# Optimization experiments

Hardware: AMD Instinct MI355X
Metric: run time of the kernel (lower is better)

The kernel has to match this reference:

```python
import jax, jax.numpy as jnp
import numpy as np

N_NODES = 100000
N_EDGES = 1600000
HID = 128
N_GRAPHS = 512
MAX_Z = 1000
NODE_VOCAB = 200000
OUT = 2
BN_EPS = 1e-5


def setup_inputs() -> dict:
    key = jax.random.key(0)
    ks = jax.random.split(key, 20)

    def w(k, shape, fan_in):
        return jax.random.normal(k, shape, dtype=jnp.float32) / np.sqrt(fan_in)

    inp = {
        "num_nodes": N_NODES,
        "z": jax.random.randint(ks[0], (N_NODES,), 0, MAX_Z),
        "edge_index": jax.random.randint(ks[1], (2, N_EDGES), 0, N_NODES),
        "batch": jnp.sort(jax.random.randint(ks[2], (N_NODES,), 0, N_GRAPHS)),
        "node_id": jax.random.randint(ks[3], (N_NODES,), 0, NODE_VOCAB),
        # parameters
        "z_emb": jax.random.normal(ks[4], (MAX_Z, HID), dtype=jnp.float32) * 0.02,
        "node_emb": jax.random.normal(ks[5], (NODE_VOCAB, HID), dtype=jnp.float32) * 0.02,
        "W0": w(ks[6], (2 * HID, HID), 2 * HID), "b0": jnp.zeros((HID,), jnp.float32),
        "W1": w(ks[7], (HID, HID), HID), "b1": jnp.zeros((HID,), jnp.float32),
        "W2": w(ks[8], (HID, HID), HID), "b2": jnp.zeros((HID,), jnp.float32),
        "mlp_W1": w(ks[9], (HID, HID), HID), "mlp_b1": jnp.zeros((HID,), jnp.float32),
        "bn_gamma": jnp.ones((HID,), jnp.float32), "bn_beta": jnp.zeros((HID,), jnp.float32),
        "mlp_W2": w(ks[10], (HID, OUT), HID), "mlp_b2": jnp.zeros((OUT,), jnp.float32),
    }
    return inp


def _gin_conv(x, src, dst, W, b, num_nodes):
    # GINConv(eps=0): out_i = Linear(x_i + sum_{j->i} x_j)
    agg = jax.ops.segment_sum(x[src], dst, num_segments=num_nodes)
    return (x + agg) @ W + b


def reference(num_nodes, z, edge_index, batch, node_id,
              z_emb, node_emb, W0, b0, W1, b1, W2, b2,
              mlp_W1, mlp_b1, bn_gamma, bn_beta, mlp_W2, mlp_b2):
    src, dst = edge_index[0], edge_index[1]
    # node features: concat(z_embedding(z), node_embedding(node_id)) -> [N, 2H]
    x = jnp.concatenate([z_emb[z], node_emb[node_id]], axis=1)

    x = jax.nn.relu(_gin_conv(x, src, dst, W0, b0, num_nodes))  # [N, H]
    x = jax.nn.relu(_gin_conv(x, src, dst, W1, b1, num_nodes))
    x = _gin_conv(x, src, dst, W2, b2, num_nodes)  # last conv: no relu

    # global mean pool over graphs
    sums = jax.ops.segment_sum(x, batch, num_segments=N_GRAPHS)  # [G, H]
    counts = jax.ops.segment_sum(jnp.ones((num_nodes,), x.dtype), batch,
                                 num_segments=N_GRAPHS)
    pooled = sums / jnp.maximum(counts, 1.0)[:, None]

    # MLP([H, H, OUT]): Linear -> BatchNorm(eval, identity stats) -> ReLU -> Linear
    h = pooled @ mlp_W1 + mlp_b1
    h = h * (bn_gamma / np.sqrt(1.0 + BN_EPS)) + bn_beta
    h = jax.nn.relu(h)
    return h @ mlp_W2 + mlp_b2  # [G, OUT]
```

## Files before the change

kernel.cpp:

```cpp
#include <hip/hip_runtime.h>

#define NN 100000
#define NE 1600000
#define HID 128
#define NG 512
#define MAXZ 1000
#define NBK 256
#define BK_S 391
#define TILE_E 4096

typedef unsigned short u16;
typedef unsigned int u32;
typedef __attribute__((ext_vector_type(8))) short bf16x8;
typedef __attribute__((ext_vector_type(4))) float f32x4;

__device__ __forceinline__ u16 bf16r(float x) {
    u32 u = __float_as_uint(x);
    u32 r = (u + 0x7fffu + ((u >> 16) & 1u)) >> 16;
    return (u16)r;
}
__device__ __forceinline__ float bflo(u32 u) { return __uint_as_float(u << 16); }
__device__ __forceinline__ float bfhi(u32 u) { return __uint_as_float(u & 0xffff0000u); }

#define ACC8(v) { \
    acc[0] += bflo((v).x); acc[1] += bfhi((v).x); \
    acc[2] += bflo((v).y); acc[3] += bfhi((v).y); \
    acc[4] += bflo((v).z); acc[5] += bfhi((v).z); \
    acc[6] += bflo((v).w); acc[7] += bfhi((v).w); }

__global__ __launch_bounds__(256) void bucket_count_kernel(const int* __restrict__ dst,
                                                           int* __restrict__ bcount) {
    __shared__ int lh[NBK];
    int t = threadIdx.x;
    lh[t] = 0;
    __syncthreads();
    int stride = gridDim.x * 256;
    for (int i = blockIdx.x * 256 + t; i < NE; i += stride)
        atomicAdd(&lh[dst[i] / BK_S], 1);
    __syncthreads();
    int v = lh[t];
    if (v) atomicAdd(&bcount[t], v);
}

__global__ __launch_bounds__(NBK) void scan_nbk_kernel(const int* __restrict__ bcount,
                                                       int* __restrict__ boff,
                                                       int* __restrict__ gcursor) {
    __shared__ int buf[NBK];
    int t = threadIdx.x;
    int v = bcount[t];
    buf[t] = v;
    __syncthreads();
    for (int d = 1; d < NBK; d <<= 1) {
        int add = (t >= d) ? buf[t - d] : 0;
        __syncthreads();
        buf[t] += add;
        __syncthreads();
    }
    int excl = buf[t] - v;
    boff[t] = excl;
    gcursor[t] = excl;
    if (t == NBK - 1) boff[NBK] = buf[NBK - 1];
}

__global__ __launch_bounds__(256) void pair_scatter_kernel(const int* __restrict__ src,
                                                           const int* __restrict__ dst,
                                                           int* __restrict__ gcursor,
                                                           u32* __restrict__ pairs) {
    __shared__ int cnt[NBK];
    __shared__ int base[NBK];
    int t = threadIdx.x;
    long tile0 = (long)blockIdx.x * TILE_E;
    cnt[t] = 0;
    __syncthreads();
    u32 val[16], br[16];
#pragma unroll
    for (int i = 0; i < 16; ++i) {
        long idx = tile0 + i * 256 + t;
        val[i] = 0xFFFFFFFFu;
        if (idx < NE) {
            int d = dst[idx];
            int b = d / BK_S;
            int r = atomicAdd(&cnt[b], 1);
            val[i] = ((u32)(d - b * BK_S) << 17) | (u32)src[idx];
            br[i] = ((u32)b << 12) | (u32)r;
        }
    }
    __syncthreads();
    int c = cnt[t];
    if (c) base[t] = atomicAdd(&gcursor[t], c);
    __syncthreads();
#pragma unroll
    for (int i = 0; i < 16; ++i) {
        if (val[i] != 0xFFFFFFFFu) {
            u32 b = br[i] >> 12, r = br[i] & 0xFFFu;
            pairs[base[b] + r] = val[i];
        }
    }
}

__global__ __launch_bounds__(256) void bucket_build_kernel(const u32* __restrict__ pairs,
                                                           const int* __restrict__ boff,
                                                           int* __restrict__ off,
                                                           int* __restrict__ csr) {
    __shared__ int lh[BK_S];
    __shared__ int ts[256];
    int b = blockIdx.x, t = threadIdx.x;
    int base = boff[b], end = boff[b + 1];
    int node0 = b * BK_S;
    for (int i = t; i < BK_S; i += 256) lh[i] = 0;
    __syncthreads();
    for (int j = base + t; j < end; j += 256)
        atomicAdd(&lh[pairs[j] >> 17], 1);
    __syncthreads();
    int i0 = t * 2, i1 = t * 2 + 1;
    int c0 = (i0 < BK_S) ? lh[i0] : 0;
    int c1 = (i1 < BK_S) ? lh[i1] : 0;
    int s = c0 + c1;
    ts[t] = s;
    __syncthreads();
    for (int d = 1; d < 256; d <<= 1) {
        int add = (t >= d) ? ts[t - d] : 0;
        __syncthreads();
        ts[t] += add;
        __syncthreads();
    }
    int e0 = base + ts[t] - s;
    int e1 = e0 + c0;
    if (i0 < BK_S) { lh[i0] = e0; int n = node0 + i0; if (n < NN) off[n] = e0; }
    if (i1 < BK_S) { lh[i1] = e1; int n = node0 + i1; if (n < NN) off[n] = e1; }
    if (b == 0 && t == 0) off[NN] = NE;
    __syncthreads();
    for (int j = base + t; j < end; j += 256) {
        u32 p = pairs[j];
        int pos = atomicAdd(&lh[p >> 17], 1);
        csr[pos] = (int)(p & 0x1FFFFu);
    }
}

__global__ __launch_bounds__(128) void wt2_kernel(const float* __restrict__ W0b, const float* __restrict__ W1,
                                                  u16* __restrict__ W0bt, u16* __restrict__ W1t) {
    int k = blockIdx.x & 127;
    int which = blockIdx.x >> 7;
    int n = threadIdx.x;
    const float* W = which ? W1 : W0b;
    u16* o = which ? W1t : W0bt;
    o[n * HID + k] = bf16r(W[k * HID + n]);
}

#define FMA4(acc, s, w) { acc.x += (s)*(w).x; acc.y += (s)*(w).y; acc.z += (s)*(w).z; acc.w += (s)*(w).w; }
__global__ __launch_bounds__(256) void gemm128_kernel(
    const float* __restrict__ X, const float* __restrict__ W,
    float* __restrict__ Y, int nrows)
{
    __shared__ float xs[32][132];
    int t = threadIdx.x;
    int row0 = blockIdx.x * 32;
    int sr = t >> 5;
    int sk = (t & 31) * 4;
#pragma unroll
    for (int p = 0; p < 4; ++p) {
        int r = p * 8 + sr;
        int grow = row0 + r;
        float4 v = make_float4(0.f, 0.f, 0.f, 0.f);
        if (grow < nrows) v = *(const float4*)(X + (long)grow * HID + sk);
        *(float4*)(&xs[r][sk]) = v;
    }
    __syncthreads();
    int cg = t & 31, rg = t >> 5;
    int c = cg * 4, r = rg * 4;
    float4 a0 = make_float4(0,0,0,0), a1 = a0, a2 = a0, a3 = a0;
    for (int k = 0; k < 128; k += 4) {
        float x0[4], x1[4], x2[4], x3[4];
        *(float4*)x0 = *(const float4*)&xs[r + 0][k];
        *(float4*)x1 = *(const float4*)&xs[r + 1][k];
        *(float4*)x2 = *(const float4*)&xs[r + 2][k];
        *(float4*)x3 = *(const float4*)&xs[r + 3][k];
#pragma unroll
        for (int j = 0; j < 4; ++j) {
            float4 w = *(const float4*)(W + (k + j) * HID + c);
            FMA4(a0, x0[j], w); FMA4(a1, x1[j], w); FMA4(a2, x2[j], w); FMA4(a3, x3[j], w);
        }
    }
    float4 accs[4] = {a0, a1, a2, a3};
#pragma unroll
    for (int i = 0; i < 4; ++i) {
        int grow = row0 + r + i;
        if (grow < nrows) *(float4*)(Y + (long)grow * HID + c) = accs[i];
    }
}

template<int SRC_BF16>
__global__ __launch_bounds__(256) void mfma_gemm_kernel(
    const void* __restrict__ Xsrc,
    const int* __restrict__ gatherIdx,
    const u16* __restrict__ Wt,
    const float* __restrict__ addTab, const int* __restrict__ addIdx,
    u16* __restrict__ Y, int nrows)
{
    __shared__ u16 Als[64][136];
    __shared__ u16 Wls[128][136];
    int t = threadIdx.x;
    int row0 = blockIdx.x * 64;

#pragma unroll
    for (int p = 0; p < 2; ++p) {
        int n = p * 64 + (t >> 2);
        int k0 = (t & 3) * 32;
        const u16* src = Wt + n * HID + k0;
        uint4 v0 = *(const uint4*)(src);
        uint4 v1 = *(const uint4*)(src + 8);
        uint4 v2 = *(const uint4*)(src + 16);
        uint4 v3 = *(const uint4*)(src + 24);
        *(uint4*)&Wls[n][k0]      = v0;
        *(uint4*)&Wls[n][k0 + 8]  = v1;
        *(uint4*)&Wls[n][k0 + 16] = v2;
        *(uint4*)&Wls[n][k0 + 24] = v3;
    }

    if (SRC_BF16) {
        const u16* X = (const u16*)Xsrc;
#pragma unroll
        for (int p = 0; p < 4; ++p) {
            int r = p * 16 + (t >> 4);
            int k0 = (t & 15) * 8;
            int grow = row0 + r;
            uint4 v = make_uint4(0, 0, 0, 0);
            if (grow < nrows) {
                long srow = gatherIdx ? (long)gatherIdx[grow] : (long)grow;
                v = *(const uint4*)(X + srow * HID + k0);
            }
            *(uint4*)&Als[r][k0] = v;
        }
    } else {
        const float* X = (const float*)Xsrc;
#pragma unroll
        for (int p = 0; p < 8; ++p) {
            int r = p * 8 + (t >> 5);
            int k0 = (t & 31) * 4;
            int grow = row0 + r;
            float4 v = make_float4(0.f, 0.f, 0.f, 0.f);
            if (grow < nrows) {
                long srow = gatherIdx ? (long)gatherIdx[grow] : (long)grow;
                v = *(const float4*)(X + srow * HID + k0);
            }
            ushort4 b;
            b.x = bf16r(v.x); b.y = bf16r(v.y); b.z = bf16r(v.z); b.w = bf16r(v.w);
            *(ushort4*)&Als[r][k0] = b;
        }
    }
    __syncthreads();

    int w = t >> 6, l = t & 63;
    int lr = l & 15, lq = l >> 4;
    f32x4 acc[8];
#pragma unroll
    for (int i = 0; i < 8; ++i) acc[i] = (f32x4){0.f, 0.f, 0.f, 0.f};

#pragma unroll
    for (int kk = 0; kk < 4; ++kk) {
        bf16x8 af = *(const bf16x8*)&Als[w * 16 + lr][kk * 32 + lq * 8];
#pragma unroll
        for (int nt = 0; nt < 8; ++nt) {
            bf16x8 bf = *(const bf16x8*)&Wls[nt * 16 + lr][kk * 32 + lq * 8];
            acc[nt] = __builtin_amdgcn_mfma_f32_16x16x32_bf16(af, bf, acc[nt], 0, 0, 0);
        }
    }

    int orow = row0 + w * 16 + lq * 4;
#pragma unroll
    for (int r = 0; r < 4; ++r) {
        int grow = orow + r;
        if (grow < nrows) {
            const float* ap = addTab ? (addTab + (long)addIdx[grow] * HID) : nullptr;
#pragma unroll
            for (int nt = 0; nt < 8; ++nt) {
                int col = nt * 16 + lr;
                float v = acc[nt][r];
                if (ap) v += ap[col];
                Y[(long)grow * HID + col] = bf16r(v);
            }
        }
    }
}

__global__ __launch_bounds__(256) void aggregate_kernel(
    const u16* __restrict__ H, u16* __restrict__ Xo,
    const int* __restrict__ off, const int* __restrict__ csr,
    const float* __restrict__ bias, int n, int doRelu)
{
    int node = blockIdx.x * 4 + (threadIdx.x >> 6);
    if (node >= n) return;
    int lane = threadIdx.x & 63;
    int g = lane >> 4, fl = lane & 15;
    int s = off[node], e = off[node + 1];

    float acc[8] = {0.f, 0.f, 0.f, 0.f, 0.f, 0.f, 0.f, 0.f};
    int j = s + g;

    for (; j + 12 < e; j += 16) {
        int i0 = csr[j];
        int i1 = csr[j + 4];
        int i2 = csr[j + 8];
        int i3 = csr[j + 12];
        uint4 v0 = *(const uint4*)(H + (long)i0 * HID + fl * 8);
        uint4 v1 = *(const uint4*)(H + (long)i1 * HID + fl * 8);
        uint4 v2 = *(const uint4*)(H + (long)i2 * HID + fl * 8);
        uint4 v3 = *(const uint4*)(H + (long)i3 * HID + fl * 8);
        ACC8(v0); ACC8(v1); ACC8(v2); ACC8(v3);
    }
    for (; j + 4 < e; j += 8) {
        int i0 = csr[j];
        int i1 = csr[j + 4];
        uint4 v0 = *(const uint4*)(H + (long)i0 * HID + fl * 8);
        uint4 v1 = *(const uint4*)(H + (long)i1 * HID + fl * 8);
        ACC8(v0); ACC8(v1);
    }
    if (j < e) {
        int i0 = csr[j];
        uint4 v0 = *(const uint4*)(H + (long)i0 * HID + fl * 8);
        ACC8(v0);
    }

#pragma unroll
    for (int i = 0; i < 8; ++i) {
        acc[i] += __shfl_xor(acc[i], 16);
        acc[i] += __shfl_xor(acc[i], 32);
    }

    if (g == 0) {
        uint4 sv = *(const uint4*)(H + (long)node * HID + fl * 8);
        float r[8];
        r[0] = acc[0] + bflo(sv.x);
        r[1] = acc[1] + bfhi(sv.x);
        r[2] = acc[2] + bflo(sv.y);
        r[3] = acc[3] + bfhi(sv.y);
        r[4] = acc[4] + bflo(sv.z);
        r[5] = acc[5] + bfhi(sv.z);
        r[6] = acc[6] + bflo(sv.w);
        r[7] = acc[7] + bfhi(sv.w);
        if (bias) {
            float4 ba = *(const float4*)(bias + fl * 8);
            float4 bb = *(const float4*)(bias + fl * 8 + 4);
            r[0] += ba.x; r[1] += ba.y; r[2] += ba.z; r[3] += ba.w;
            r[4] += bb.x; r[5] += bb.y; r[6] += bb.z; r[7] += bb.w;
        }
        if (doRelu) {
#pragma unroll
            for (int i = 0; i < 8; ++i) r[i] = fmaxf(r[i], 0.f);
        }
        uint4 ov;
        ov.x = (u32)bf16r(r[0]) | ((u32)bf16r(r[1]) << 16);
        ov.y = (u32)bf16r(r[2]) | ((u32)bf16r(r[3]) << 16);
        ov.z = (u32)bf16r(r[4]) | ((u32)bf16r(r[5]) << 16);
        ov.w = (u32)bf16r(r[6]) | ((u32)bf16r(r[7]) << 16);
        *(uint4*)(Xo + (long)node * HID + fl * 8) = ov;
    }
}

__global__ __launch_bounds__(256) void pool_kernel(const u16* __restrict__ X, const int* __restrict__ batch,
                                                   int n, float* __restrict__ pooled) {
    __shared__ float red[4][HID];
    int g = blockIdx.x;
    int t = threadIdx.x;
    int grp = t >> 4, fl = t & 15;
    int lo = 0, hi = n;
    while (lo < hi) { int m = (lo + hi) >> 1; if (batch[m] < g) lo = m + 1; else hi = m; }
    int s = lo;
    lo = 0; hi = n;
    while (lo < hi) { int m = (lo + hi) >> 1; if (batch[m] < g + 1) lo = m + 1; else hi = m; }
    int e = lo;

    float acc[8] = {0.f, 0.f, 0.f, 0.f, 0.f, 0.f, 0.f, 0.f};
    for (int i = s + grp; i < e; i += 16) {
        uint4 v = *(const uint4*)(X + (long)i * HID + fl * 8);
        ACC8(v);
    }
#pragma unroll
    for (int i = 0; i < 8; ++i) {
        acc[i] += __shfl_xor(acc[i], 16);
        acc[i] += __shfl_xor(acc[i], 32);
    }
    int w = t >> 6, lane = t & 63;
    if (lane < 16) {
#pragma unroll
        for (int i = 0; i < 8; ++i) red[w][lane * 8 + i] = acc[i];
    }
    __syncthreads();
    if (t < HID) {
        float v = red[0][t] + red[1][t] + red[2][t] + red[3][t];
        float cnt = (float)(e - s);
        pooled[g * HID + t] = v / fmaxf(cnt, 1.f);
    }
}

__global__ __launch_bounds__(128) void mlp_kernel(
    const float* __restrict__ poolT, const float* __restrict__ W2f, const float* __restrict__ b2,
    const float* __restrict__ W1, const float* __restrict__ b1,
    const float* __restrict__ gamma, const float* __restrict__ beta,
    const float* __restrict__ mW2, const float* __restrict__ mb2, float* __restrict__ out)
{
    int g = blockIdx.x, t = threadIdx.x;
    __shared__ float pt[HID];
    __shared__ float p[HID];
    __shared__ float red[4];
    pt[t] = poolT[g * HID + t];
    __syncthreads();
    float pv = b2[t];
    for (int k = 0; k < HID; ++k) pv += pt[k] * W2f[k * HID + t];
    p[t] = pv;
    __syncthreads();
    float acc = b1[t];
    for (int k = 0; k < HID; ++k) acc += p[k] * W1[k * HID + t];
    const float inv = 1.0f / sqrtf(1.0f + 1e-5f);
    acc = acc * (gamma[t] * inv) + beta[t];
    acc = fmaxf(acc, 0.f);
    float v0 = acc * mW2[t * 2 + 0];
    float v1 = acc * mW2[t * 2 + 1];
    for (int d = 32; d > 0; d >>= 1) { v0 += __shfl_down(v0, d); v1 += __shfl_down(v1, d); }
    int w = t >> 6, lane = t & 63;
    if (lane == 0) { red[w * 2] = v0; red[w * 2 + 1] = v1; }
    __syncthreads();
    if (t == 0) {
        out[g * 2 + 0] = red[0] + red[2] + mb2[0];
        out[g * 2 + 1] = red[1] + red[3] + mb2[1];
    }
}

extern "C" void kernel_launch(void* const* d_in, const int* in_sizes, int n_in,
                              void* d_out, int out_size, void* d_ws, size_t ws_size,
                              hipStream_t stream) {
    const int*   z        = (const int*)d_in[1];
    const int*   ei       = (const int*)d_in[2];
    const int*   batch    = (const int*)d_in[3];
    const int*   node_id  = (const int*)d_in[4];
    const float* z_emb    = (const float*)d_in[5];
    const float* node_emb = (const float*)d_in[6];
    const float* W0  = (const float*)d_in[7];
    const float* b0  = (const float*)d_in[8];
    const float* W1  = (const float*)d_in[9];
    const float* b1  = (const float*)d_in[10];
    const float* W2  = (const float*)d_in[11];
    const float* b2  = (const float*)d_in[12];
    const float* mW1 = (const float*)d_in[13];
    const float* mb1 = (const float*)d_in[14];
    const float* gam = (const float*)d_in[15];
    const float* bet = (const float*)d_in[16];
    const float* mW2 = (const float*)d_in[17];
    const float* mb2 = (const float*)d_in[18];
    float* out = (float*)d_out;

    const int* srcArr = ei;
    const int* dstArr = ei + NE;

    char* ws = (char*)d_ws;
    size_t o = 0;
    auto alloc = [&](size_t bytes) { char* p = ws + o; o += (bytes + 255) & ~(size_t)255; return p; };
    u16*   A      = (u16*)alloc((size_t)NN * HID * 2);
    u16*   B      = (u16*)alloc((size_t)NN * HID * 2);
    float* zW     = (float*)alloc((size_t)MAXZ * HID * 4);
    u16*   W0bt   = (u16*)alloc((size_t)HID * HID * 2);
    u16*   W1t    = (u16*)alloc((size_t)HID * HID * 2);
    int*   bcount = (int*)alloc((size_t)NBK * 4);
    int*   boff   = (int*)alloc((size_t)(NBK + 1) * 4);
    int*   gcur   = (int*)alloc((size_t)NBK * 4);
    u32*   pairs  = (u32*)alloc((size_t)NE * 4);
    int*   off    = (int*)alloc((size_t)(NN + 1) * 4);
    int*   csr    = (int*)alloc((size_t)NE * 4);
    float* poolT  = (float*)alloc((size_t)NG * HID * 4);
    (void)ws_size;

    hipMemsetAsync(bcount, 0, (size_t)NBK * 4, stream);
    bucket_count_kernel<<<1024, 256, 0, stream>>>(dstArr, bcount);
    scan_nbk_kernel<<<1, NBK, 0, stream>>>(bcount, boff, gcur);
    pair_scatter_kernel<<<(NE + TILE_E - 1) / TILE_E, 256, 0, stream>>>(srcArr, dstArr, gcur, pairs);
    bucket_build_kernel<<<NBK, 256, 0, stream>>>(pairs, boff, off, csr);

    wt2_kernel<<<2 * HID, HID, 0, stream>>>(W0 + HID * HID, W1, W0bt, W1t);

    gemm128_kernel<<<(MAXZ + 31) / 32, 256, 0, stream>>>(z_emb, W0, zW, MAXZ);

    const int GB = (NN + 63) / 64;
    mfma_gemm_kernel<0><<<GB, 256, 0, stream>>>(node_emb, node_id, W0bt, zW, z, B, NN);
    aggregate_kernel<<<NN / 4, 256, 0, stream>>>(B, A, off, csr, b0, NN, 1);
    mfma_gemm_kernel<1><<<GB, 256, 0, stream>>>(A, nullptr, W1t, nullptr, nullptr, B, NN);
    aggregate_kernel<<<NN / 4, 256, 0, stream>>>(B, A, off, csr, b1, NN, 1);
    aggregate_kernel<<<NN / 4, 256, 0, stream>>>(A, B, off, csr, nullptr, NN, 0);

    pool_kernel<<<NG, 256, 0, stream>>>(B, batch, NN, poolT);
    mlp_kernel<<<NG, 128, 0, stream>>>(poolT, W2, b2, mW1, mb1, gam, bet, mW2, mb2, out);
}
```

Before: 361.7 us.

## Fuse final GIN aggregation into graph pooling via CSR edge sums

Drops the last aggregate kernel. Mean pooling is linear, so each graph's sum of (x_i + agg_i) is computed directly from its nodes' features plus all in-edge source features, found through the CSR range of that graph's contiguous nodes. This removes one full pass over the edges into a node buffer plus its write and re-read. Parallelism now drops to one block per graph (512 blocks), each walking roughly 3000 edges. Also halves the edge-scatter tile size and makes the bias load unconditional, since every remaining caller passes a bias.

```diff
diff --git a/kernel.cpp b/kernel.cpp
--- a/kernel.cpp
+++ b/kernel.cpp
@@ -7,7 +7,7 @@
 #define MAXZ 1000
 #define NBK 256
 #define BK_S 391
-#define TILE_E 4096
+#define TILE_E 2048
 
 typedef unsigned short u16;
 typedef unsigned int u32;
@@ -72,9 +72,9 @@
     long tile0 = (long)blockIdx.x * TILE_E;
     cnt[t] = 0;
     __syncthreads();
-    u32 val[16], br[16];
-#pragma unroll
-    for (int i = 0; i < 16; ++i) {
+    u32 val[8], br[8];
+#pragma unroll
+    for (int i = 0; i < 8; ++i) {
         long idx = tile0 + i * 256 + t;
         val[i] = 0xFFFFFFFFu;
         if (idx < NE) {
@@ -90,7 +90,7 @@
     if (c) base[t] = atomicAdd(&gcursor[t], c);
     __syncthreads();
 #pragma unroll
-    for (int i = 0; i < 16; ++i) {
+    for (int i = 0; i < 8; ++i) {
         if (val[i] != 0xFFFFFFFFu) {
             u32 b = br[i] >> 12, r = br[i] & 0xFFFu;
             pairs[base[b] + r] = val[i];
@@ -329,21 +329,17 @@
 
     if (g == 0) {
         uint4 sv = *(const uint4*)(H + (long)node * HID + fl * 8);
+        float4 ba = *(const float4*)(bias + fl * 8);
+        float4 bb = *(const float4*)(bias + fl * 8 + 4);
         float r[8];
-        r[0] = acc[0] + bflo(sv.x);
-        r[1] = acc[1] + bfhi(sv.x);
-        r[2] = acc[2] + bflo(sv.y);
-        r[3] = acc[3] + bfhi(sv.y);
-        r[4] = acc[4] + bflo(sv.z);
-        r[5] = acc[5] + bfhi(sv.z);
-        r[6] = acc[6] + bflo(sv.w);
-        r[7] = acc[7] + bfhi(sv.w);
-        if (bias) {
-            float4 ba = *(const float4*)(bias + fl * 8);
-            float4 bb = *(const float4*)(bias + fl * 8 + 4);
-            r[0] += ba.x; r[1] += ba.y; r[2] += ba.z; r[3] += ba.w;
-            r[4] += bb.x; r[5] += bb.y; r[6] += bb.z; r[7] += bb.w;
-        }
+        r[0] = acc[0] + bflo(sv.x) + ba.x;
+        r[1] = acc[1] + bfhi(sv.x) + ba.y;
+        r[2] = acc[2] + bflo(sv.y) + ba.z;
+        r[3] = acc[3] + bfhi(sv.y) + ba.w;
+        r[4] = acc[4] + bflo(sv.z) + bb.x;
+        r[5] = acc[5] + bfhi(sv.z) + bb.y;
+        r[6] = acc[6] + bflo(sv.w) + bb.z;
+        r[7] = acc[7] + bfhi(sv.w) + bb.w;
         if (doRelu) {
 #pragma unroll
             for (int i = 0; i < 8; ++i) r[i] = fmaxf(r[i], 0.f);
@@ -357,24 +353,46 @@
     }
 }
 
-__global__ __launch_bounds__(256) void pool_kernel(const u16* __restrict__ X, const int* __restrict__ batch,
-                                                   int n, float* __restrict__ pooled) {
+__global__ __launch_bounds__(256) void edgepool_kernel(
+    const u16* __restrict__ X, const int* __restrict__ batch,
+    const int* __restrict__ off, const int* __restrict__ csr,
+    float* __restrict__ pooled)
+{
     __shared__ float red[4][HID];
     int g = blockIdx.x;
     int t = threadIdx.x;
     int grp = t >> 4, fl = t & 15;
-    int lo = 0, hi = n;
+    int lo = 0, hi = NN;
     while (lo < hi) { int m = (lo + hi) >> 1; if (batch[m] < g) lo = m + 1; else hi = m; }
-    int s = lo;
-    lo = 0; hi = n;
+    int ns = lo;
+    lo = 0; hi = NN;
     while (lo < hi) { int m = (lo + hi) >> 1; if (batch[m] < g + 1) lo = m + 1; else hi = m; }
-    int e = lo;
+    int ne = lo;
+    int es = off[ns], ee = off[ne];
 
     float acc[8] = {0.f, 0.f, 0.f, 0.f, 0.f, 0.f, 0.f, 0.f};
-    for (int i = s + grp; i < e; i += 16) {
+    for (int i = ns + grp; i < ne; i += 16) {
         uint4 v = *(const uint4*)(X + (long)i * HID + fl * 8);
         ACC8(v);
     }
+    int j = es + grp;
+    for (; j + 48 < ee; j += 64) {
+        int i0 = csr[j];
+        int i1 = csr[j + 16];
+        int i2 = csr[j + 32];
+        int i3 = csr[j + 48];
+        uint4 v0 = *(const uint4*)(X + (long)i0 * HID + fl * 8);
+        uint4 v1 = *(const uint4*)(X + (long)i1 * HID + fl * 8);
+        uint4 v2 = *(const uint4*)(X + (long)i2 * HID + fl * 8);
+        uint4 v3 = *(const uint4*)(X + (long)i3 * HID + fl * 8);
+        ACC8(v0); ACC8(v1); ACC8(v2); ACC8(v3);
+    }
+    for (; j < ee; j += 16) {
+        int i0 = csr[j];
+        uint4 v0 = *(const uint4*)(X + (long)i0 * HID + fl * 8);
+        ACC8(v0);
+    }
+
 #pragma unroll
     for (int i = 0; i < 8; ++i) {
         acc[i] += __shfl_xor(acc[i], 16);
@@ -388,7 +406,7 @@
     __syncthreads();
     if (t < HID) {
         float v = red[0][t] + red[1][t] + red[2][t] + red[3][t];
-        float cnt = (float)(e - s);
+        float cnt = (float)(ne - ns);
         pooled[g * HID + t] = v / fmaxf(cnt, 1.f);
     }
 }
@@ -484,8 +502,6 @@
     aggregate_kernel<<<NN / 4, 256, 0, stream>>>(B, A, off, csr, b0, NN, 1);
     mfma_gemm_kernel<1><<<GB, 256, 0, stream>>>(A, nullptr, W1t, nullptr, nullptr, B, NN);
     aggregate_kernel<<<NN / 4, 256, 0, stream>>>(B, A, off, csr, b1, NN, 1);
-    aggregate_kernel<<<NN / 4, 256, 0, stream>>>(A, B, off, csr, nullptr, NN, 0);
-
-    pool_kernel<<<NG, 256, 0, stream>>>(B, batch, NN, poolT);
+    edgepool_kernel<<<NG, 256, 0, stream>>>(A, batch, off, csr, poolT);
     mlp_kernel<<<NG, 128, 0, stream>>>(poolT, W2, b2, mW1, mb1, gam, bet, mW2, mb2, out);
 }
```

New measurement: 361.6 us. Within noise of the previous version (-0.0%).
